# Kernel optimization log

Hardware: AMD Instinct MI355X
Metric: run time of the kernel (lower is better)

Reference implementation:

```python
import jax, jax.numpy as jnp
import numpy as np

B, T, C = 4, 2048, 2048
H, D, L = 16, 128, 512


def _rope(x, cos, sin):
    # x: [B, T, H, D]; cos/sin: [T, D//2]; consecutive-pair complex rotation
    x2 = x.reshape(*x.shape[:-1], -1, 2)
    x0, x1 = x2[..., 0], x2[..., 1]
    c = cos[None, :, None, :]
    s = sin[None, :, None, :]
    o0 = x0 * c - x1 * s
    o1 = x0 * s + x1 * c
    return jnp.stack([o0, o1], axis=-1).reshape(x.shape)


def setup_inputs() -> dict:
    key = jax.random.key(0)
    ks = jax.random.split(key, 8)
    x = jax.random.normal(ks[0], (B, T, C), dtype=jnp.float32)
    # rotary table, theta = 10000
    inv_freq = 1.0 / (10000.0 ** (np.arange(0, D, 2, dtype=np.float32) / D))
    ang = np.outer(np.arange(T, dtype=np.float32), inv_freq)
    freqs_cos = jnp.asarray(np.cos(ang), dtype=jnp.float32)
    freqs_sin = jnp.asarray(np.sin(ang), dtype=jnp.float32)
    sc = 0.02
    wq = sc * jax.random.normal(ks[1], (H * D, C), dtype=jnp.float32)
    wkv_down = sc * jax.random.normal(ks[2], (L, C), dtype=jnp.float32)
    wk_up = sc * jax.random.normal(ks[3], (D, L), dtype=jnp.float32)
    wv_up = sc * jax.random.normal(ks[4], (D, L), dtype=jnp.float32)
    wo = sc * jax.random.normal(ks[5], (C, H * D), dtype=jnp.float32)
    return {"x": x, "freqs_cos": freqs_cos, "freqs_sin": freqs_sin,
            "wq": wq, "wkv_down": wkv_down, "wk_up": wk_up,
            "wv_up": wv_up, "wo": wo}


def reference(x, freqs_cos, freqs_sin, wq, wkv_down, wk_up, wv_up, wo):
    Bc, Tc, Cc = x.shape
    # query projection -> [B, T, H, D]
    q = jnp.einsum('btc,ec->bte', x, wq).reshape(Bc, Tc, H, D)
    # shared latent KV: [B, T, L]
    kv_latent = jnp.einsum('btc,lc->btl', x, wkv_down)
    # up-project to single shared head: [B, T, D]
    k = jnp.einsum('btl,dl->btd', kv_latent, wk_up)
    v = jnp.einsum('btl,dl->btd', kv_latent, wv_up)
    # RoPE on q (per head) and k (single shared head)
    q = _rope(q, freqs_cos, freqs_sin)
    k = _rope(k[:, :, None, :], freqs_cos, freqs_sin)[:, :, 0, :]
    # causal SDPA; k/v are shared across heads (MLA) so avoid expanding them
    scale = 1.0 / jnp.sqrt(jnp.asarray(D, dtype=x.dtype))
    scores = jnp.einsum('bthd,bsd->bhts', q, k) * scale  # [B, H, T, S]
    causal = jnp.tril(jnp.ones((Tc, Tc), dtype=bool))
    scores = jnp.where(causal[None, None, :, :], scores, jnp.finfo(x.dtype).min)
    probs = jax.nn.softmax(scores, axis=-1)
    y = jnp.einsum('bhts,bsd->bthd', probs, v).reshape(Bc, Tc, H * D)
    return jnp.einsum('bte,ce->btc', y, wo)
```

## Files before the change

kernel.cpp:

```cpp
#include <hip/hip_runtime.h>
#include <hip/hip_bf16.h>
#include <cstddef>

#define BB 4
#define TT 2048
#define CC 2048
#define HH 16
#define DD 128
#define LL 512

typedef _Float16 f16;
typedef f16 f16x2 __attribute__((ext_vector_type(2)));
typedef f16 f16x4 __attribute__((ext_vector_type(4)));
typedef f16 f16x8 __attribute__((ext_vector_type(8)));
typedef float f32x4 __attribute__((ext_vector_type(4)));

__device__ __forceinline__ void async_load16(void* lptr, const void* gptr) {
  __builtin_amdgcn_global_load_lds(
      (const __attribute__((address_space(1))) unsigned int*)gptr,
      (__attribute__((address_space(3))) unsigned int*)lptr, 16, 0, 0);
}

template <int EPI>
__global__ __launch_bounds__(512, 2) void mla_gemm_256(
    const f16* __restrict__ A, const f16* __restrict__ B,
    void* __restrict__ Cv, int M, int N, int K,
    const float* __restrict__ cosb, const float* __restrict__ sinb) {
  __shared__ __align__(16) f16 smem[2][2][256 * 64];

  const int tid = threadIdx.x;
  const int lane = tid & 63;
  const int w = tid >> 6;
  const int lnm = lane & 15, quad = lane >> 4;
  const int wm = w >> 2, wn = w & 3;

  const int nwg = gridDim.x;
  const int bid0 = blockIdx.x;
  const int q8 = nwg >> 3, r8 = nwg & 7;
  const int xcd = bid0 & 7, lid = bid0 >> 3;
  const int wg =
      (xcd < r8 ? xcd * (q8 + 1) : r8 * (q8 + 1) + (xcd - r8) * q8) + lid;
  const int ntc = N >> 8;
  const int m0 = (wg / ntc) * 256;
  const int n0 = (wg % ntc) * 256;

  const int srow = tid >> 3;
  const int sch = (tid & 7) ^ ((tid >> 3) & 7);
  const f16* Ag = A + (size_t)(m0 + srow) * K + sch * 8;
  const f16* Bg = B + (size_t)(n0 + srow) * K + sch * 8;

  auto stage = [&](int bi, int k0, int h) {
    const int mat = h >> 1;
    const int rb = (h & 1) * 128;
    const f16* g = (mat ? Bg : Ag) + (size_t)rb * K + k0;
    f16* l = &smem[bi][mat][rb * 64 + tid * 8];
    async_load16(l, g);
    async_load16(l + 4096, g + (size_t)64 * K);
  };

  const int rx8 = lnm & 7;
  auto rdA = [&](const f16* Ab, int i, int ks) -> f16x8 {
    return *(const f16x8*)&Ab[(wm * 128 + i * 16 + lnm) * 64 +
                              (((ks * 4 + quad) ^ rx8) * 8)];
  };
  auto rdB = [&](const f16* Bb, int j, int ks) -> f16x8 {
    return *(const f16x8*)&Bb[(wn * 64 + j * 16 + lnm) * 64 +
                              (((ks * 4 + quad) ^ rx8) * 8)];
  };

  f32x4 acc[8][4] = {};

  const int NT = K >> 6;

  stage(0, 0, 0);
  stage(0, 0, 1);
  stage(0, 0, 2);
  stage(0, 0, 3);
  stage(1, 64, 0);
  asm volatile("s_waitcnt vmcnt(2)" ::: "memory");
  __builtin_amdgcn_s_barrier();

  for (int t = 0; t < NT; ++t) {
    const int bi = t & 1;
    const f16* Ab = smem[bi][0];
    const f16* Bb = smem[bi][1];
    const int k1 = (t + 1 < NT ? t + 1 : t) << 6;
    const int k2 = (t + 2 < NT ? t + 2 : t) << 6;

    f16x8 Ar[4][2], Br[2][2];

#pragma unroll
    for (int i = 0; i < 4; i++)
#pragma unroll
      for (int ks = 0; ks < 2; ks++) Ar[i][ks] = rdA(Ab, i, ks);
#pragma unroll
    for (int j = 0; j < 2; j++)
#pragma unroll
      for (int ks = 0; ks < 2; ks++) Br[j][ks] = rdB(Bb, j, ks);
    stage(bi ^ 1, k1, 1);
    __builtin_amdgcn_s_barrier();
    asm volatile("s_waitcnt lgkmcnt(0)" ::: "memory");
    __builtin_amdgcn_s_setprio(1);
#pragma unroll
    for (int i = 0; i < 4; i++)
#pragma unroll
      for (int j = 0; j < 2; j++)
#pragma unroll
        for (int ks = 0; ks < 2; ks++)
          acc[i][j] = __builtin_amdgcn_mfma_f32_16x16x32_f16(
              Ar[i][ks], Br[j][ks], acc[i][j], 0, 0, 0);
    __builtin_amdgcn_s_setprio(0);
    __builtin_amdgcn_s_barrier();

#pragma unroll
    for (int j = 0; j < 2; j++)
#pragma unroll
      for (int ks = 0; ks < 2; ks++) Br[j][ks] = rdB(Bb, 2 + j, ks);
    stage(bi ^ 1, k1, 2);
    __builtin_amdgcn_s_barrier();
    asm volatile("s_waitcnt lgkmcnt(0)" ::: "memory");
    __builtin_amdgcn_s_setprio(1);
#pragma unroll
    for (int i = 0; i < 4; i++)
#pragma unroll
      for (int j = 0; j < 2; j++)
#pragma unroll
        for (int ks = 0; ks < 2; ks++)
          acc[i][2 + j] = __builtin_amdgcn_mfma_f32_16x16x32_f16(
              Ar[i][ks], Br[j][ks], acc[i][2 + j], 0, 0, 0);
    __builtin_amdgcn_s_setprio(0);
    __builtin_amdgcn_s_barrier();

#pragma unroll
    for (int i = 0; i < 4; i++)
#pragma unroll
      for (int ks = 0; ks < 2; ks++) Ar[i][ks] = rdA(Ab, 4 + i, ks);
    stage(bi ^ 1, k1, 3);
    __builtin_amdgcn_s_barrier();
    asm volatile("s_waitcnt lgkmcnt(0)" ::: "memory");
    __builtin_amdgcn_s_setprio(1);
#pragma unroll
    for (int i = 0; i < 4; i++)
#pragma unroll
      for (int j = 0; j < 2; j++)
#pragma unroll
        for (int ks = 0; ks < 2; ks++)
          acc[4 + i][2 + j] = __builtin_amdgcn_mfma_f32_16x16x32_f16(
              Ar[i][ks], Br[j][ks], acc[4 + i][2 + j], 0, 0, 0);
    __builtin_amdgcn_s_setprio(0);
    __builtin_amdgcn_s_barrier();

#pragma unroll
    for (int j = 0; j < 2; j++)
#pragma unroll
      for (int ks = 0; ks < 2; ks++) Br[j][ks] = rdB(Bb, j, ks);
    stage(bi, k2, 0);
    __builtin_amdgcn_s_barrier();
    asm volatile("s_waitcnt lgkmcnt(0)" ::: "memory");
    __builtin_amdgcn_s_setprio(1);
#pragma unroll
    for (int i = 0; i < 4; i++)
#pragma unroll
      for (int j = 0; j < 2; j++)
#pragma unroll
        for (int ks = 0; ks < 2; ks++)
          acc[4 + i][j] = __builtin_amdgcn_mfma_f32_16x16x32_f16(
              Ar[i][ks], Br[j][ks], acc[4 + i][j], 0, 0, 0);
    __builtin_amdgcn_s_setprio(0);
    asm volatile("s_waitcnt vmcnt(2)" ::: "memory");
    __builtin_amdgcn_s_barrier();
  }

  asm volatile("s_waitcnt vmcnt(0)" ::: "memory");

  if constexpr (EPI == 0) {
    float* C = (float*)Cv;
#pragma unroll
    for (int i = 0; i < 8; i++)
#pragma unroll
      for (int r = 0; r < 4; r++) {
        float* crow = C + (size_t)(m0 + wm * 128 + i * 16 + quad * 4 + r) * N +
                      n0 + wn * 64 + lnm;
#pragma unroll
        for (int j = 0; j < 4; j++) crow[j * 16] = acc[i][j][r];
      }
  } else {
    f16* C = (f16*)Cv;
    const float SCLQ = 0.1275174280f;
#pragma unroll
    for (int i = 0; i < 8; i++)
#pragma unroll
      for (int r = 0; r < 4; r++) {
        const int m = m0 + wm * 128 + i * 16 + quad * 4 + r;
        const int t = m & (TT - 1);
#pragma unroll
        for (int j = 0; j < 4; j++) {
          const int col = n0 + wn * 64 + j * 16 + lnm;
          float v = acc[i][j][r];
          float u = __shfl_xor(v, 1, 64);
          const int fi = (col & (DD - 1)) >> 1;
          const float ct = cosb[t * (DD / 2) + fi];
          const float st2 = sinb[t * (DD / 2) + fi];
          const float o =
              (lnm & 1) ? (u * st2 + v * ct) : (v * ct - u * st2);
          C[(size_t)m * N + col] = (f16)(o * SCLQ);
        }
      }
  }
}

__global__ __launch_bounds__(256) void mla_gemm_mfma(
    const f16* __restrict__ A, const f16* __restrict__ B,
    float* __restrict__ C, int M, int N, int K) {
  __shared__ f16 As[128 * 32];
  __shared__ f16 Bs[128 * 32];

  const int tid = threadIdx.x;
  const int lane = tid & 63;
  const int w = tid >> 6;
  const int lnm = lane & 15, quad = lane >> 4;
  const int wm = w >> 1, wn = w & 1;
  const int m0 = blockIdx.y * 128;
  const int n0 = blockIdx.x * 128;

  const int srow = tid >> 2;
  const int skoff = (tid & 3) * 8;

  f32x4 acc[4][4] = {};

  for (int k0 = 0; k0 < K; k0 += 32) {
    const f16* ag = A + (size_t)(m0 + srow) * K + k0 + skoff;
    const f16* bg = B + (size_t)(n0 + srow) * K + k0 + skoff;
    async_load16(&As[(size_t)tid * 8], ag);
    async_load16(&As[(size_t)(256 + tid) * 8], ag + (size_t)64 * K);
    async_load16(&Bs[(size_t)tid * 8], bg);
    async_load16(&Bs[(size_t)(256 + tid) * 8], bg + (size_t)64 * K);
    __syncthreads();

    f16x8 af[4], bf[4];
#pragma unroll
    for (int i = 0; i < 4; i++)
      af[i] = *(const f16x8*)&As[(wm * 64 + i * 16 + lnm) * 32 + quad * 8];
#pragma unroll
    for (int j = 0; j < 4; j++)
      bf[j] = *(const f16x8*)&Bs[(wn * 64 + j * 16 + lnm) * 32 + quad * 8];
#pragma unroll
    for (int i = 0; i < 4; i++)
#pragma unroll
      for (int j = 0; j < 4; j++)
        acc[i][j] = __builtin_amdgcn_mfma_f32_16x16x32_f16(af[i], bf[j],
                                                           acc[i][j], 0, 0, 0);
    __syncthreads();
  }

#pragma unroll
  for (int i = 0; i < 4; i++)
#pragma unroll
    for (int r = 0; r < 4; r++) {
      float* crow = C + (size_t)(m0 + wm * 64 + i * 16 + quad * 4 + r) * N +
                    n0 + wn * 64 + lnm;
#pragma unroll
      for (int j = 0; j < 4; j++) crow[j * 16] = acc[i][j][r];
    }
}

__global__ __launch_bounds__(256) void mla_cvt_f16(
    const float4* __restrict__ in, f16* __restrict__ out, int n4) {
  int i = blockIdx.x * 256 + threadIdx.x;
  if (i >= n4) return;
  float4 v = in[i];
  f16x4 r = {(f16)v.x, (f16)v.y, (f16)v.z, (f16)v.w};
  *(f16x4*)(out + (size_t)i * 4) = r;
}

__global__ __launch_bounds__(256) void mla_rope_cvt(
    const float2* __restrict__ x, f16* __restrict__ o,
    const float* __restrict__ cosb, const float* __restrict__ sinb,
    int Hh, float scale, int total) {
  int idx = blockIdx.x * blockDim.x + threadIdx.x;
  if (idx >= total) return;
  const int Dh = DD / 2;
  int i = idx % Dh;
  int t = (idx / (Dh * Hh)) % TT;
  float c = cosb[t * Dh + i];
  float s = sinb[t * Dh + i];
  float2 v = x[idx];
  f16x2 r;
  r.x = (f16)((v.x * c - v.y * s) * scale);
  r.y = (f16)((v.x * s + v.y * c) * scale);
  *(f16x2*)(o + (size_t)idx * 2) = r;
}

__global__ __launch_bounds__(256) void mla_transpose_v(
    const float* __restrict__ v, f16* __restrict__ vt) {
  __shared__ float tl[32][33];
  const int b = blockIdx.z;
  const int t0 = blockIdx.x * 32;
  const int d0 = blockIdx.y * 32;
  const int tx = threadIdx.x & 31;
  const int ty = threadIdx.x >> 5;
#pragma unroll
  for (int k = 0; k < 4; k++)
    tl[ty + 8 * k][tx] = v[((size_t)(b * TT + t0 + ty + 8 * k)) * DD + d0 + tx];
  __syncthreads();
#pragma unroll
  for (int k = 0; k < 4; k++)
    vt[((size_t)(b * DD + d0 + ty + 8 * k)) * TT + t0 + tx] =
        (f16)tl[tx][ty + 8 * k];
}

__global__ __launch_bounds__(512, 2) void mla_flash2(
    const f16* __restrict__ qh, const f16* __restrict__ kh,
    const f16* __restrict__ vth, f16* __restrict__ y) {
  __shared__ f16 Ks[2][64 * 128];
  __shared__ f16 Vs[2][128 * 64];

  const int tid = threadIdx.x;
  const int lane = tid & 63;
  const int w = tid >> 6;
  const int lnm = lane & 15, quad = lane >> 4;

  const int bid = blockIdx.x;
  const int qt = (TT / 256 - 1) - (bid >> 6);
  const int bh = bid & 63;
  const int b = bh >> 4, h = bh & 15;
  const int q0b = qt * 256;
  const int q0 = q0b + w * 32;

  f16x8 qf[2][4];
#pragma unroll
  for (int qnb = 0; qnb < 2; qnb++) {
    const f16* qrow =
        qh + ((size_t)(b * TT + q0 + qnb * 16 + lnm) * HH + h) * DD;
#pragma unroll
    for (int c = 0; c < 4; c++)
      qf[qnb][c] = *(const f16x8*)(qrow + c * 32 + quad * 8);
  }

  f32x4 O[2][8] = {};
  float l_acc[2] = {0.f, 0.f};

  const int nst = (q0b + 256) / 64;
  const int wmax = q0 + 31;
  const f16* kbase = kh + (size_t)b * TT * DD;
  const f16* vbase = vth + (size_t)b * DD * TT;

  const int ks_row = tid >> 4;
  const int ks_col = ((tid & 15) ^ ((tid >> 4) & 15)) * 8;
  const int vs_row = tid >> 3;
  const int vs_col = ((tid & 7) ^ ((tid >> 3) & 7)) * 8;

  auto stage = [&](int buf, int st) {
    const int s0 = st * 64;
#pragma unroll
    for (int i = 0; i < 2; i++)
      async_load16(&Ks[buf][(size_t)(i * 512 + tid) * 8],
                   kbase + (size_t)(s0 + i * 32 + ks_row) * DD + ks_col);
#pragma unroll
    for (int i = 0; i < 2; i++)
      async_load16(&Vs[buf][(size_t)(i * 512 + tid) * 8],
                   vbase + (size_t)(i * 64 + vs_row) * TT + s0 + vs_col);
  };

  stage(0, 0);
  __syncthreads();

  for (int st = 0; st < nst; st++) {
    const int cur = st & 1;
    const int s0 = st * 64;
    if (st + 1 < nst) stage(cur ^ 1, st + 1);

    if (s0 <= wmax) {
      const f16* Kc = Ks[cur];
      const f16* Vc = Vs[cur];

      f32x4 S[2][4] = {};
      __builtin_amdgcn_s_setprio(1);
#pragma unroll
      for (int sb = 0; sb < 4; sb++) {
        const int sl = sb * 16 + lnm;
#pragma unroll
        for (int c = 0; c < 4; c++) {
          f16x8 ka =
              *(const f16x8*)&Kc[sl * 128 + ((c * 4 + quad) ^ lnm) * 8];
          S[0][sb] = __builtin_amdgcn_mfma_f32_16x16x32_f16(ka, qf[0][c],
                                                            S[0][sb], 0, 0, 0);
          S[1][sb] = __builtin_amdgcn_mfma_f32_16x16x32_f16(ka, qf[1][c],
                                                            S[1][sb], 0, 0, 0);
        }
      }
      __builtin_amdgcn_s_setprio(0);

      f16x8 P8[2][2];
      const bool domask = (s0 + 63 > q0);
      if (!domask) {
#pragma unroll
        for (int qnb = 0; qnb < 2; qnb++) {
          float lp = 0.f;
#pragma unroll
          for (int sb = 0; sb < 4; sb++)
#pragma unroll
            for (int j = 0; j < 4; j++) {
              float p = __builtin_amdgcn_exp2f(S[qnb][sb][j]);
              lp += p;
              P8[qnb][sb >> 1][(sb & 1) * 4 + j] = (f16)p;
            }
          l_acc[qnb] += lp;
        }
      } else {
#pragma unroll
        for (int qnb = 0; qnb < 2; qnb++) {
          const int m_abs = q0 + qnb * 16 + lnm;
          float lp = 0.f;
#pragma unroll
          for (int sb = 0; sb < 4; sb++) {
            const int srow = s0 + sb * 16 + quad * 4;
#pragma unroll
            for (int j = 0; j < 4; j++) {
              float p = __builtin_amdgcn_exp2f(S[qnb][sb][j]);
              if (srow + j > m_abs) p = 0.f;
              lp += p;
              P8[qnb][sb >> 1][(sb & 1) * 4 + j] = (f16)p;
            }
          }
          l_acc[qnb] += lp;
        }
      }

      __builtin_amdgcn_s_setprio(1);
#pragma unroll
      for (int c = 0; c < 2; c++) {
        const int chlo = c * 4 + (quad >> 1);
        const int soff = (quad & 1) * 4;
#pragma unroll
        for (int db = 0; db < 8; db++) {
          const int d = db * 16 + lnm;
          const f16* vrow = &Vc[d * 64];
          f16x4 vlo = *(const f16x4*)&vrow[((chlo ^ (d & 7)) * 8) + soff];
          f16x4 vhi =
              *(const f16x4*)&vrow[(((chlo + 2) ^ (d & 7)) * 8) + soff];
          f16x8 vb;
#pragma unroll
          for (int j = 0; j < 4; j++) {
            vb[j] = vlo[j];
            vb[4 + j] = vhi[j];
          }
          O[0][db] = __builtin_amdgcn_mfma_f32_16x16x32_f16(P8[0][c], vb,
                                                            O[0][db], 0, 0, 0);
          O[1][db] = __builtin_amdgcn_mfma_f32_16x16x32_f16(P8[1][c], vb,
                                                            O[1][db], 0, 0, 0);
        }
      }
      __builtin_amdgcn_s_setprio(0);
    }
    __syncthreads();
  }

#pragma unroll
  for (int qnb = 0; qnb < 2; qnb++) {
    float l = l_acc[qnb];
    l += __shfl_xor(l, 16, 64);
    l += __shfl_xor(l, 32, 64);
    l_acc[qnb] = l;
  }

#pragma unroll
  for (int qnb = 0; qnb < 2; qnb++) {
    float linv[4];
#pragma unroll
    for (int r = 0; r < 4; r++)
      linv[r] = 1.f / __shfl(l_acc[qnb], quad * 4 + r, 64);
#pragma unroll
    for (int db = 0; db < 8; db++)
#pragma unroll
      for (int r = 0; r < 4; r++) {
        size_t off =
            ((size_t)(b * TT + q0 + qnb * 16 + quad * 4 + r) * HH + h) * DD +
            db * 16 + lnm;
        y[off] = (f16)(O[qnb][db][r] * linv[r]);
      }
  }
}

extern "C" void kernel_launch(void* const* d_in, const int* in_sizes, int n_in,
                              void* d_out, int out_size, void* d_ws,
                              size_t ws_size, hipStream_t stream) {
  const float* x      = (const float*)d_in[0];
  const float* fcos   = (const float*)d_in[1];
  const float* fsin   = (const float*)d_in[2];
  const float* wq     = (const float*)d_in[3];
  const float* wkv_dn = (const float*)d_in[4];
  const float* wk_up  = (const float*)d_in[5];
  const float* wv_up  = (const float*)d_in[6];
  const float* wo     = (const float*)d_in[7];
  float* out = (float*)d_out;

  const int M = BB * TT;

  float* ws = (float*)d_ws;
  float* qbuf   = ws;
  float* kv     = qbuf + (size_t)M * CC;
  float* kk     = kv + (size_t)M * LL;
  float* vv     = kk + (size_t)M * DD;
  f16*   xh     = (f16*)(vv + (size_t)M * DD);
  f16*   wqh    = xh + (size_t)M * CC;
  f16*   wdownh = wqh + (size_t)CC * CC;
  f16*   wkuph  = wdownh + (size_t)LL * CC;
  f16*   wvuph  = wkuph + (size_t)DD * LL;
  f16*   woh    = wvuph + (size_t)DD * LL;
  f16*   kvh    = woh + (size_t)CC * CC;
  f16*   khb    = kvh + (size_t)M * LL;
  f16*   vth    = khb + (size_t)M * DD;
  f16*   qh     = (f16*)qbuf;
  f16*   yh     = qh + (size_t)M * CC;

  dim3 blk(256);

  mla_cvt_f16<<<(M * CC / 4 + 255) / 256, blk, 0, stream>>>(
      (const float4*)x, xh, M * CC / 4);
  mla_cvt_f16<<<(CC * CC / 4 + 255) / 256, blk, 0, stream>>>(
      (const float4*)wq, wqh, CC * CC / 4);
  mla_cvt_f16<<<(LL * CC / 4 + 255) / 256, blk, 0, stream>>>(
      (const float4*)wkv_dn, wdownh, LL * CC / 4);
  mla_cvt_f16<<<(DD * LL / 4 + 255) / 256, blk, 0, stream>>>(
      (const float4*)wk_up, wkuph, DD * LL / 4);
  mla_cvt_f16<<<(DD * LL / 4 + 255) / 256, blk, 0, stream>>>(
      (const float4*)wv_up, wvuph, DD * LL / 4);
  mla_cvt_f16<<<(CC * CC / 4 + 255) / 256, blk, 0, stream>>>(
      (const float4*)wo, woh, CC * CC / 4);

  mla_gemm_256<1><<<dim3((M / 256) * (CC / 256)), dim3(512), 0, stream>>>(
      xh, wqh, qh, M, CC, CC, fcos, fsin);
  mla_gemm_mfma<<<dim3(LL / 128, M / 128), blk, 0, stream>>>(
      xh, wdownh, kv, M, LL, CC);

  mla_cvt_f16<<<(M * LL / 4 + 255) / 256, blk, 0, stream>>>(
      (const float4*)kv, kvh, M * LL / 4);
  mla_gemm_mfma<<<dim3(DD / 128, M / 128), blk, 0, stream>>>(
      kvh, wkuph, kk, M, DD, LL);
  mla_gemm_mfma<<<dim3(DD / 128, M / 128), blk, 0, stream>>>(
      kvh, wvuph, vv, M, DD, LL);

  {
    int total_k = BB * TT * (DD / 2);
    mla_rope_cvt<<<(total_k + 255) / 256, blk, 0, stream>>>(
        (const float2*)kk, khb, fcos, fsin, 1, 1.0f, total_k);
  }

  mla_transpose_v<<<dim3(TT / 32, DD / 32, BB), blk, 0, stream>>>(vv, vth);

  mla_flash2<<<dim3(BB * HH * (TT / 256)), dim3(512), 0, stream>>>(
      qh, khb, vth, yh);

  mla_gemm_256<0><<<dim3((M / 256) * (CC / 256)), dim3(512), 0, stream>>>(
      yh, woh, out, M, CC, CC, nullptr, nullptr);
}
```

Baseline: 465.9 us.

## Software-pipeline QK^T one tile ahead in flash kernel and merge K/V up-projections

```diff
diff --git a/kernel.cpp b/kernel.cpp
--- a/kernel.cpp
+++ b/kernel.cpp
@@ -276,15 +276,16 @@
 __global__ __launch_bounds__(256) void mla_rope_cvt(
     const float2* __restrict__ x, f16* __restrict__ o,
     const float* __restrict__ cosb, const float* __restrict__ sinb,
-    int Hh, float scale, int total) {
+    int ld2, float scale, int total) {
   int idx = blockIdx.x * blockDim.x + threadIdx.x;
   if (idx >= total) return;
   const int Dh = DD / 2;
-  int i = idx % Dh;
-  int t = (idx / (Dh * Hh)) % TT;
+  int i = idx & (Dh - 1);
+  int m = idx >> 6;
+  int t = m & (TT - 1);
   float c = cosb[t * Dh + i];
   float s = sinb[t * Dh + i];
-  float2 v = x[idx];
+  float2 v = x[(size_t)m * ld2 + i];
   f16x2 r;
   r.x = (f16)((v.x * c - v.y * s) * scale);
   r.y = (f16)((v.x * s + v.y * c) * scale);
@@ -292,7 +293,7 @@
 }
 
 __global__ __launch_bounds__(256) void mla_transpose_v(
-    const float* __restrict__ v, f16* __restrict__ vt) {
+    const float* __restrict__ v, f16* __restrict__ vt, int ldv) {
   __shared__ float tl[32][33];
   const int b = blockIdx.z;
   const int t0 = blockIdx.x * 32;
@@ -301,7 +302,8 @@
   const int ty = threadIdx.x >> 5;
 #pragma unroll
   for (int k = 0; k < 4; k++)
-    tl[ty + 8 * k][tx] = v[((size_t)(b * TT + t0 + ty + 8 * k)) * DD + d0 + tx];
+    tl[ty + 8 * k][tx] =
+        v[((size_t)(b * TT + t0 + ty + 8 * k)) * ldv + d0 + tx];
   __syncthreads();
 #pragma unroll
   for (int k = 0; k < 4; k++)
@@ -338,6 +340,7 @@
   }
 
   f32x4 O[2][8] = {};
+  f32x4 S[2][4];
   float l_acc[2] = {0.f, 0.f};
 
   const int nst = (q0b + 256) / 64;
@@ -350,84 +353,99 @@
   const int vs_row = tid >> 3;
   const int vs_col = ((tid & 7) ^ ((tid >> 3) & 7)) * 8;
 
-  auto stage = [&](int buf, int st) {
+  auto stageK = [&](int buf, int st) {
     const int s0 = st * 64;
 #pragma unroll
     for (int i = 0; i < 2; i++)
       async_load16(&Ks[buf][(size_t)(i * 512 + tid) * 8],
                    kbase + (size_t)(s0 + i * 32 + ks_row) * DD + ks_col);
+  };
+  auto stageV = [&](int buf, int st) {
+    const int s0 = st * 64;
 #pragma unroll
     for (int i = 0; i < 2; i++)
       async_load16(&Vs[buf][(size_t)(i * 512 + tid) * 8],
                    vbase + (size_t)(i * 64 + vs_row) * TT + s0 + vs_col);
   };
 
-  stage(0, 0);
+  auto qk = [&](const f16* Kc) {
+    const f32x4 z = {0.f, 0.f, 0.f, 0.f};
+#pragma unroll
+    for (int qnb = 0; qnb < 2; qnb++)
+#pragma unroll
+      for (int sb = 0; sb < 4; sb++) S[qnb][sb] = z;
+#pragma unroll
+    for (int sb = 0; sb < 4; sb++) {
+      const int sl = sb * 16 + lnm;
+#pragma unroll
+      for (int c = 0; c < 4; c++) {
+        f16x8 ka = *(const f16x8*)&Kc[sl * 128 + ((c * 4 + quad) ^ lnm) * 8];
+        S[0][sb] = __builtin_amdgcn_mfma_f32_16x16x32_f16(ka, qf[0][c],
+                                                          S[0][sb], 0, 0, 0);
+        S[1][sb] = __builtin_amdgcn_mfma_f32_16x16x32_f16(ka, qf[1][c],
+                                                          S[1][sb], 0, 0, 0);
+      }
+    }
+  };
+
+  stageK(0, 0);
+  stageV(0, 0);
   __syncthreads();
+  stageK(1, 1 < nst ? 1 : 0);
+  qk(Ks[0]);
+  __syncthreads();
 
   for (int st = 0; st < nst; st++) {
-    const int cur = st & 1;
-    const int s0 = st * 64;
-    if (st + 1 < nst) stage(cur ^ 1, st + 1);
-
-    if (s0 <= wmax) {
-      const f16* Kc = Ks[cur];
+    const int cur = st & 1, nxt = cur ^ 1;
+    const int s0c = st * 64;
+    stageK(cur, st + 2 < nst ? st + 2 : nst - 1);
+    stageV(nxt, st + 1 < nst ? st + 1 : nst - 1);
+
+    const bool act = (s0c <= wmax);
+    f16x8 P8[2][2];
+    if (act) {
+      const bool domask = (s0c + 63 > q0);
+#pragma unroll
+      for (int qnb = 0; qnb < 2; qnb++) {
+        const int m_abs = q0 + qnb * 16 + lnm;
+        float lp = 0.f;
+#pragma unroll
+        for (int sb = 0; sb < 4; sb++) {
+          const int srow = s0c + sb * 16 + quad * 4;
+          float p[4];
+#pragma unroll
+          for (int j = 0; j < 4; j++) {
+            float e = __builtin_amdgcn_exp2f(S[qnb][sb][j]);
+            if (domask && (srow + j > m_abs)) e = 0.f;
+            p[j] = e;
+            lp += e;
+          }
+          f16x2* pp = (f16x2*)&P8[qnb][sb >> 1];
+#if __has_builtin(__builtin_amdgcn_cvt_pkrtz)
+          {
+            auto h0 = __builtin_amdgcn_cvt_pkrtz(p[0], p[1]);
+            auto h1 = __builtin_amdgcn_cvt_pkrtz(p[2], p[3]);
+            pp[(sb & 1) * 2 + 0] = *(const f16x2*)&h0;
+            pp[(sb & 1) * 2 + 1] = *(const f16x2*)&h1;
+          }
+#else
+          {
+            f16x2 h0 = {(f16)p[0], (f16)p[1]};
+            f16x2 h1 = {(f16)p[2], (f16)p[3]};
+            pp[(sb & 1) * 2 + 0] = h0;
+            pp[(sb & 1) * 2 + 1] = h1;
+          }
+#endif
+        }
+        l_acc[qnb] += lp;
+      }
+    }
+
+    __builtin_amdgcn_s_setprio(1);
+    if ((st + 1) * 64 <= wmax) qk(Ks[nxt]);
+
+    if (act) {
       const f16* Vc = Vs[cur];
-
-      f32x4 S[2][4] = {};
-      __builtin_amdgcn_s_setprio(1);
-#pragma unroll
-      for (int sb = 0; sb < 4; sb++) {
-        const int sl = sb * 16 + lnm;
-#pragma unroll
-        for (int c = 0; c < 4; c++) {
-          f16x8 ka =
-              *(const f16x8*)&Kc[sl * 128 + ((c * 4 + quad) ^ lnm) * 8];
-          S[0][sb] = __builtin_amdgcn_mfma_f32_16x16x32_f16(ka, qf[0][c],
-                                                            S[0][sb], 0, 0, 0);
-          S[1][sb] = __builtin_amdgcn_mfma_f32_16x16x32_f16(ka, qf[1][c],
-                                                            S[1][sb], 0, 0, 0);
-        }
-      }
-      __builtin_amdgcn_s_setprio(0);
-
-      f16x8 P8[2][2];
-      const bool domask = (s0 + 63 > q0);
-      if (!domask) {
-#pragma unroll
-        for (int qnb = 0; qnb < 2; qnb++) {
-          float lp = 0.f;
-#pragma unroll
-          for (int sb = 0; sb < 4; sb++)
-#pragma unroll
-            for (int j = 0; j < 4; j++) {
-              float p = __builtin_amdgcn_exp2f(S[qnb][sb][j]);
-              lp += p;
-              P8[qnb][sb >> 1][(sb & 1) * 4 + j] = (f16)p;
-            }
-          l_acc[qnb] += lp;
-        }
-      } else {
-#pragma unroll
-        for (int qnb = 0; qnb < 2; qnb++) {
-          const int m_abs = q0 + qnb * 16 + lnm;
-          float lp = 0.f;
-#pragma unroll
-          for (int sb = 0; sb < 4; sb++) {
-            const int srow = s0 + sb * 16 + quad * 4;
-#pragma unroll
-            for (int j = 0; j < 4; j++) {
-              float p = __builtin_amdgcn_exp2f(S[qnb][sb][j]);
-              if (srow + j > m_abs) p = 0.f;
-              lp += p;
-              P8[qnb][sb >> 1][(sb & 1) * 4 + j] = (f16)p;
-            }
-          }
-          l_acc[qnb] += lp;
-        }
-      }
-
-      __builtin_amdgcn_s_setprio(1);
 #pragma unroll
       for (int c = 0; c < 2; c++) {
         const int chlo = c * 4 + (quad >> 1);
@@ -451,8 +469,8 @@
                                                             O[1][db], 0, 0, 0);
         }
       }
-      __builtin_amdgcn_s_setprio(0);
     }
+    __builtin_amdgcn_s_setprio(0);
     __syncthreads();
   }
 
@@ -500,14 +518,12 @@
   float* ws = (float*)d_ws;
   float* qbuf   = ws;
   float* kv     = qbuf + (size_t)M * CC;
-  float* kk     = kv + (size_t)M * LL;
-  float* vv     = kk + (size_t)M * DD;
-  f16*   xh     = (f16*)(vv + (size_t)M * DD);
+  float* kkvv   = kv + (size_t)M * LL;
+  f16*   xh     = (f16*)(kkvv + (size_t)M * 256);
   f16*   wqh    = xh + (size_t)M * CC;
   f16*   wdownh = wqh + (size_t)CC * CC;
-  f16*   wkuph  = wdownh + (size_t)LL * CC;
-  f16*   wvuph  = wkuph + (size_t)DD * LL;
-  f16*   woh    = wvuph + (size_t)DD * LL;
+  f16*   wkvuph = wdownh + (size_t)LL * CC;
+  f16*   woh    = wkvuph + (size_t)256 * LL;
   f16*   kvh    = woh + (size_t)CC * CC;
   f16*   khb    = kvh + (size_t)M * LL;
   f16*   vth    = khb + (size_t)M * DD;
@@ -523,9 +539,9 @@
   mla_cvt_f16<<<(LL * CC / 4 + 255) / 256, blk, 0, stream>>>(
       (const float4*)wkv_dn, wdownh, LL * CC / 4);
   mla_cvt_f16<<<(DD * LL / 4 + 255) / 256, blk, 0, stream>>>(
-      (const float4*)wk_up, wkuph, DD * LL / 4);
+      (const float4*)wk_up, wkvuph, DD * LL / 4);
   mla_cvt_f16<<<(DD * LL / 4 + 255) / 256, blk, 0, stream>>>(
-      (const float4*)wv_up, wvuph, DD * LL / 4);
+      (const float4*)wv_up, wkvuph + (size_t)DD * LL, DD * LL / 4);
   mla_cvt_f16<<<(CC * CC / 4 + 255) / 256, blk, 0, stream>>>(
       (const float4*)wo, woh, CC * CC / 4);
 
@@ -536,18 +552,17 @@
 
   mla_cvt_f16<<<(M * LL / 4 + 255) / 256, blk, 0, stream>>>(
       (const float4*)kv, kvh, M * LL / 4);
-  mla_gemm_mfma<<<dim3(DD / 128, M / 128), blk, 0, stream>>>(
-      kvh, wkuph, kk, M, DD, LL);
-  mla_gemm_mfma<<<dim3(DD / 128, M / 128), blk, 0, stream>>>(
-      kvh, wvuph, vv, M, DD, LL);
+  mla_gemm_mfma<<<dim3(256 / 128, M / 128), blk, 0, stream>>>(
+      kvh, wkvuph, kkvv, M, 256, LL);
 
   {
     int total_k = BB * TT * (DD / 2);
     mla_rope_cvt<<<(total_k + 255) / 256, blk, 0, stream>>>(
-        (const float2*)kk, khb, fcos, fsin, 1, 1.0f, total_k);
-  }
-
-  mla_transpose_v<<<dim3(TT / 32, DD / 32, BB), blk, 0, stream>>>(vv, vth);
+        (const float2*)kkvv, khb, fcos, fsin, 128, 1.0f, total_k);
+  }
+
+  mla_transpose_v<<<dim3(TT / 32, DD / 32, BB), blk, 0, stream>>>(
+      kkvv + 128, vth, 256);
 
   mla_flash2<<<dim3(BB * HH * (TT / 256)), dim3(512), 0, stream>>>(
       qh, khb, vth, yh);
```

Measured after the change: 455.3 us. -2.3%, faster.

## Pre-pack K/V into MFMA fragment order and merge K/V up-projection GEMMs

Applied to the files above, without the earlier changes.

```diff
diff --git a/kernel.cpp b/kernel.cpp
--- a/kernel.cpp
+++ b/kernel.cpp
@@ -273,47 +273,66 @@
   *(f16x4*)(out + (size_t)i * 4) = r;
 }
 
-__global__ __launch_bounds__(256) void mla_rope_cvt(
-    const float2* __restrict__ x, f16* __restrict__ o,
+__global__ __launch_bounds__(256) void mla_rope_k(
+    const float2* __restrict__ x, f16* __restrict__ khp,
     const float* __restrict__ cosb, const float* __restrict__ sinb,
-    int Hh, float scale, int total) {
+    int ld2, int total) {
   int idx = blockIdx.x * blockDim.x + threadIdx.x;
   if (idx >= total) return;
-  const int Dh = DD / 2;
-  int i = idx % Dh;
-  int t = (idx / (Dh * Hh)) % TT;
-  float c = cosb[t * Dh + i];
-  float s = sinb[t * Dh + i];
-  float2 v = x[idx];
+  const int i = idx & 63;
+  const int m = idx >> 6;
+  const int t = m & (TT - 1);
+  const int b = m >> 11;
+  float c = cosb[t * 64 + i];
+  float s = sinb[t * 64 + i];
+  float2 v = x[(size_t)m * ld2 + i];
   f16x2 r;
-  r.x = (f16)((v.x * c - v.y * s) * scale);
-  r.y = (f16)((v.x * s + v.y * c) * scale);
-  *(f16x2*)(o + (size_t)idx * 2) = r;
-}
-
-__global__ __launch_bounds__(256) void mla_transpose_v(
-    const float* __restrict__ v, f16* __restrict__ vt) {
-  __shared__ float tl[32][33];
+  r.x = (f16)(v.x * c - v.y * s);
+  r.y = (f16)(v.x * s + v.y * c);
+  const int st = t >> 6, sl = t & 63;
+  const int cq = i >> 2, e = (i & 3) * 2;
+  size_t off = (((size_t)(b * 32 + st) * 16 + cq) * 64 + sl) * 8 + e;
+  *(f16x2*)(khp + off) = r;
+}
+
+__global__ __launch_bounds__(256) void mla_fragv(
+    const float* __restrict__ v, f16* __restrict__ vtp, int ldv) {
+  __shared__ f16 tl[64][128];
   const int b = blockIdx.z;
-  const int t0 = blockIdx.x * 32;
-  const int d0 = blockIdx.y * 32;
-  const int tx = threadIdx.x & 31;
-  const int ty = threadIdx.x >> 5;
-#pragma unroll
-  for (int k = 0; k < 4; k++)
-    tl[ty + 8 * k][tx] = v[((size_t)(b * TT + t0 + ty + 8 * k)) * DD + d0 + tx];
+  const int st = blockIdx.x;
+  const int t = threadIdx.x;
+
+  const int dl = (t & 31) * 4;
+#pragma unroll
+  for (int r = 0; r < 8; r++) {
+    const int s = r * 8 + (t >> 5);
+    float4 val = *(const float4*)&v[((size_t)(b * TT + st * 64 + s)) * ldv + dl];
+    f16x4 h = {(f16)val.x, (f16)val.y, (f16)val.z, (f16)val.w};
+    *(f16x4*)&tl[s][dl] = h;
+  }
   __syncthreads();
-#pragma unroll
-  for (int k = 0; k < 4; k++)
-    vt[((size_t)(b * DD + d0 + ty + 8 * k)) * TT + t0 + tx] =
-        (f16)tl[tx][ty + 8 * k];
+
+  f16* outb = vtp + (size_t)(b * 32 + st) * 8192;
+#pragma unroll
+  for (int k = 0; k < 4; k++) {
+    const int cd = k * 256 + t;
+    const int cq2 = cd >> 7, d = cd & 127;
+    const int c = cq2 >> 2, quad = cq2 & 3;
+    f16x8 o;
+#pragma unroll
+    for (int e = 0; e < 8; e++) {
+      const int s = c * 32 + quad * 4 + ((e >> 2) << 4) + (e & 3);
+      o[e] = tl[s][d];
+    }
+    *(f16x8*)&outb[(size_t)cd * 8] = o;
+  }
 }
 
 __global__ __launch_bounds__(512, 2) void mla_flash2(
-    const f16* __restrict__ qh, const f16* __restrict__ kh,
-    const f16* __restrict__ vth, f16* __restrict__ y) {
-  __shared__ f16 Ks[2][64 * 128];
-  __shared__ f16 Vs[2][128 * 64];
+    const f16* __restrict__ qh, const f16* __restrict__ khp,
+    const f16* __restrict__ vtp, f16* __restrict__ y) {
+  __shared__ __align__(16) f16 Ks[2][8192];
+  __shared__ __align__(16) f16 Vs[2][8192];
 
   const int tid = threadIdx.x;
   const int lane = tid & 63;
@@ -342,53 +361,51 @@
 
   const int nst = (q0b + 256) / 64;
   const int wmax = q0 + 31;
-  const f16* kbase = kh + (size_t)b * TT * DD;
-  const f16* vbase = vth + (size_t)b * DD * TT;
-
-  const int ks_row = tid >> 4;
-  const int ks_col = ((tid & 15) ^ ((tid >> 4) & 15)) * 8;
-  const int vs_row = tid >> 3;
-  const int vs_col = ((tid & 7) ^ ((tid >> 3) & 7)) * 8;
-
-  auto stage = [&](int buf, int st) {
-    const int s0 = st * 64;
-#pragma unroll
-    for (int i = 0; i < 2; i++)
-      async_load16(&Ks[buf][(size_t)(i * 512 + tid) * 8],
-                   kbase + (size_t)(s0 + i * 32 + ks_row) * DD + ks_col);
-#pragma unroll
-    for (int i = 0; i < 2; i++)
-      async_load16(&Vs[buf][(size_t)(i * 512 + tid) * 8],
-                   vbase + (size_t)(i * 64 + vs_row) * TT + s0 + vs_col);
+  const f16* kpb = khp + (size_t)b * 32 * 8192;
+  const f16* vpb = vtp + (size_t)b * 32 * 8192;
+
+  auto stageK = [&](int buf, int st) {
+    const f16* g = kpb + (size_t)st * 8192 + (size_t)tid * 8;
+    async_load16(&Ks[buf][(size_t)tid * 8], g);
+    async_load16(&Ks[buf][(size_t)(512 + tid) * 8], g + 4096);
   };
-
-  stage(0, 0);
+  auto stageV = [&](int buf, int st) {
+    const f16* g = vpb + (size_t)st * 8192 + (size_t)tid * 8;
+    async_load16(&Vs[buf][(size_t)tid * 8], g);
+    async_load16(&Vs[buf][(size_t)(512 + tid) * 8], g + 4096);
+  };
+
+  const int kbo = quad * 512 + lnm * 8;
+  const int vbo = quad * 1024 + lnm * 8;
+
+  stageK(0, 0);
+  stageV(0, 0);
   __syncthreads();
 
   for (int st = 0; st < nst; st++) {
     const int cur = st & 1;
     const int s0 = st * 64;
-    if (st + 1 < nst) stage(cur ^ 1, st + 1);
+    if (st + 1 < nst) {
+      stageK(cur ^ 1, st + 1);
+      stageV(cur ^ 1, st + 1);
+    }
 
     if (s0 <= wmax) {
-      const f16* Kc = Ks[cur];
-      const f16* Vc = Vs[cur];
+      const f16* kl = &Ks[cur][kbo];
+      const f16* vl = &Vs[cur][vbo];
 
       f32x4 S[2][4] = {};
       __builtin_amdgcn_s_setprio(1);
 #pragma unroll
-      for (int sb = 0; sb < 4; sb++) {
-        const int sl = sb * 16 + lnm;
+      for (int sb = 0; sb < 4; sb++)
 #pragma unroll
         for (int c = 0; c < 4; c++) {
-          f16x8 ka =
-              *(const f16x8*)&Kc[sl * 128 + ((c * 4 + quad) ^ lnm) * 8];
+          f16x8 ka = *(const f16x8*)&kl[c * 2048 + sb * 128];
           S[0][sb] = __builtin_amdgcn_mfma_f32_16x16x32_f16(ka, qf[0][c],
                                                             S[0][sb], 0, 0, 0);
           S[1][sb] = __builtin_amdgcn_mfma_f32_16x16x32_f16(ka, qf[1][c],
                                                             S[1][sb], 0, 0, 0);
         }
-      }
       __builtin_amdgcn_s_setprio(0);
 
       f16x8 P8[2][2];
@@ -429,28 +446,15 @@
 
       __builtin_amdgcn_s_setprio(1);
 #pragma unroll
-      for (int c = 0; c < 2; c++) {
-        const int chlo = c * 4 + (quad >> 1);
-        const int soff = (quad & 1) * 4;
+      for (int c = 0; c < 2; c++)
 #pragma unroll
         for (int db = 0; db < 8; db++) {
-          const int d = db * 16 + lnm;
-          const f16* vrow = &Vc[d * 64];
-          f16x4 vlo = *(const f16x4*)&vrow[((chlo ^ (d & 7)) * 8) + soff];
-          f16x4 vhi =
-              *(const f16x4*)&vrow[(((chlo + 2) ^ (d & 7)) * 8) + soff];
-          f16x8 vb;
-#pragma unroll
-          for (int j = 0; j < 4; j++) {
-            vb[j] = vlo[j];
-            vb[4 + j] = vhi[j];
-          }
+          f16x8 vb = *(const f16x8*)&vl[c * 4096 + db * 128];
           O[0][db] = __builtin_amdgcn_mfma_f32_16x16x32_f16(P8[0][c], vb,
                                                             O[0][db], 0, 0, 0);
           O[1][db] = __builtin_amdgcn_mfma_f32_16x16x32_f16(P8[1][c], vb,
                                                             O[1][db], 0, 0, 0);
         }
-      }
       __builtin_amdgcn_s_setprio(0);
     }
     __syncthreads();
@@ -500,17 +504,15 @@
   float* ws = (float*)d_ws;
   float* qbuf   = ws;
   float* kv     = qbuf + (size_t)M * CC;
-  float* kk     = kv + (size_t)M * LL;
-  float* vv     = kk + (size_t)M * DD;
-  f16*   xh     = (f16*)(vv + (size_t)M * DD);
+  float* kkvv   = kv + (size_t)M * LL;
+  f16*   xh     = (f16*)(kkvv + (size_t)M * 256);
   f16*   wqh    = xh + (size_t)M * CC;
   f16*   wdownh = wqh + (size_t)CC * CC;
-  f16*   wkuph  = wdownh + (size_t)LL * CC;
-  f16*   wvuph  = wkuph + (size_t)DD * LL;
-  f16*   woh    = wvuph + (size_t)DD * LL;
+  f16*   wkvuph = wdownh + (size_t)LL * CC;
+  f16*   woh    = wkvuph + (size_t)256 * LL;
   f16*   kvh    = woh + (size_t)CC * CC;
-  f16*   khb    = kvh + (size_t)M * LL;
-  f16*   vth    = khb + (size_t)M * DD;
+  f16*   khp    = kvh + (size_t)M * LL;
+  f16*   vtp    = khp + (size_t)M * DD;
   f16*   qh     = (f16*)qbuf;
   f16*   yh     = qh + (size_t)M * CC;
 
@@ -523,9 +525,9 @@
   mla_cvt_f16<<<(LL * CC / 4 + 255) / 256, blk, 0, stream>>>(
       (const float4*)wkv_dn, wdownh, LL * CC / 4);
   mla_cvt_f16<<<(DD * LL / 4 + 255) / 256, blk, 0, stream>>>(
-      (const float4*)wk_up, wkuph, DD * LL / 4);
+      (const float4*)wk_up, wkvuph, DD * LL / 4);
   mla_cvt_f16<<<(DD * LL / 4 + 255) / 256, blk, 0, stream>>>(
-      (const float4*)wv_up, wvuph, DD * LL / 4);
+      (const float4*)wv_up, wkvuph + (size_t)DD * LL, DD * LL / 4);
   mla_cvt_f16<<<(CC * CC / 4 + 255) / 256, blk, 0, stream>>>(
       (const float4*)wo, woh, CC * CC / 4);
 
@@ -536,21 +538,19 @@
 
   mla_cvt_f16<<<(M * LL / 4 + 255) / 256, blk, 0, stream>>>(
       (const float4*)kv, kvh, M * LL / 4);
-  mla_gemm_mfma<<<dim3(DD / 128, M / 128), blk, 0, stream>>>(
-      kvh, wkuph, kk, M, DD, LL);
-  mla_gemm_mfma<<<dim3(DD / 128, M / 128), blk, 0, stream>>>(
-      kvh, wvuph, vv, M, DD, LL);
+  mla_gemm_mfma<<<dim3(256 / 128, M / 128), blk, 0, stream>>>(
+      kvh, wkvuph, kkvv, M, 256, LL);
 
   {
     int total_k = BB * TT * (DD / 2);
-    mla_rope_cvt<<<(total_k + 255) / 256, blk, 0, stream>>>(
-        (const float2*)kk, khb, fcos, fsin, 1, 1.0f, total_k);
-  }
-
-  mla_transpose_v<<<dim3(TT / 32, DD / 32, BB), blk, 0, stream>>>(vv, vth);
+    mla_rope_k<<<(total_k + 255) / 256, blk, 0, stream>>>(
+        (const float2*)kkvv, khp, fcos, fsin, 128, total_k);
+  }
+
+  mla_fragv<<<dim3(TT / 64, 1, BB), blk, 0, stream>>>(kkvv + 128, vtp, 256);
 
   mla_flash2<<<dim3(BB * HH * (TT / 256)), dim3(512), 0, stream>>>(
-      qh, khb, vth, yh);
+      qh, khp, vtp, yh);
 
   mla_gemm_256<0><<<dim3((M / 256) * (CC / 256)), dim3(512), 0, stream>>>(
       yh, woh, out, M, CC, CC, nullptr, nullptr);
```

Measured after the change: 454.8 us. 2.4% less time.
